# Kernel optimization log

Hardware: AMD Instinct MI355X
Metric: run time of the kernel (lower is better)

## Reference

```python
import jax, jax.numpy as jnp
import numpy as np
import math

D_MODEL = 768
NUM_HEADS = 12


def setup_inputs() -> dict:
    key = jax.random.key(0)
    ks = jax.random.split(key, 5)
    B, S, D = 2, 2048, D_MODEL
    scale = 1.0 / math.sqrt(D)
    x = jax.random.normal(ks[0], (B, S, D), dtype=jnp.float32)
    Wq = jax.random.normal(ks[1], (D, D), dtype=jnp.float32) * scale
    Wk = jax.random.normal(ks[2], (D, D), dtype=jnp.float32) * scale
    Wv = jax.random.normal(ks[3], (D, D), dtype=jnp.float32) * scale
    Wo = jax.random.normal(ks[4], (D, D), dtype=jnp.float32) * scale
    return {"x": x, "Wq": Wq, "Wk": Wk, "Wv": Wv, "Wo": Wo}


def _mhsa(x, Wq, Wk, Wv, Wo):
    B, S, D = x.shape
    H = NUM_HEADS
    hd = D // H
    # Linear(in, out) with weight [out, in]: y = x @ W^T
    q = x @ Wq.T
    k = x @ Wk.T
    v = x @ Wv.T
    # [B, S, H, hd] -> [B, H, S, hd]
    q = q.reshape(B, S, H, hd).transpose(0, 2, 1, 3)
    k = k.reshape(B, S, H, hd).transpose(0, 2, 1, 3)
    v = v.reshape(B, S, H, hd).transpose(0, 2, 1, 3)
    scores = jnp.einsum("bhqd,bhkd->bhqk", q, k) / jnp.sqrt(jnp.float32(hd))
    causal = jnp.tril(jnp.ones((S, S), dtype=bool))  # True where allowed
    scores = jnp.where(causal, scores, -jnp.inf)
    probs = jax.nn.softmax(scores, axis=-1)
    o = jnp.einsum("bhqk,bhkd->bhqd", probs, v)
    o = o.transpose(0, 2, 1, 3).reshape(B, S, D)
    return o @ Wo.T


def reference(x, Wq, Wk, Wv, Wo):
    return _mhsa(x, Wq, Wk, Wv, Wo)
```

## Files before the change

### kernel.cpp

```cpp
#include <hip/hip_runtime.h>
#include <math.h>

#define NHEAD 12
#define HD    64
#define SEQ   2048
#define BATCH 2
#define DM    768

typedef unsigned short u16;
typedef __attribute__((ext_vector_type(8))) short bf16x8;
typedef __attribute__((ext_vector_type(8))) unsigned short u16x8;
typedef __attribute__((ext_vector_type(4))) float f32x4;

__device__ __forceinline__ u16 f2bf(float f) {
    unsigned u = __builtin_bit_cast(unsigned, f);
    return (u16)((u + 0x7fffu + ((u >> 16) & 1u)) >> 16);
}
__device__ __forceinline__ bf16x8 as_bf16x8(uint4 v) { return __builtin_bit_cast(bf16x8, v); }
__device__ __forceinline__ u16x8  as_u16x8(uint4 v)  { return __builtin_bit_cast(u16x8, v); }
__device__ __forceinline__ f32x4 mfma16(bf16x8 a, bf16x8 b, f32x4 c) {
    return __builtin_amdgcn_mfma_f32_16x16x32_bf16(a, b, c, 0, 0, 0);
}

__global__ void cvt4(const float* __restrict__ s, u16* __restrict__ d, int n4) {
    int i = blockIdx.x * blockDim.x + threadIdx.x;
    if (i < n4) {
        float4 v = ((const float4*)s)[i];
        ushort4 o;
        o.x = f2bf(v.x); o.y = f2bf(v.y); o.z = f2bf(v.z); o.w = f2bf(v.w);
        ((ushort4*)d)[i] = o;
    }
}

__global__ __launch_bounds__(256)
void qkv_mfma(const u16* __restrict__ X,
              const u16* __restrict__ Wq, const u16* __restrict__ Wk,
              const u16* __restrict__ Wv,
              u16* __restrict__ Q, u16* __restrict__ K, u16* __restrict__ V)
{
    const u16* W = blockIdx.z == 0 ? Wq : blockIdx.z == 1 ? Wk : Wv;
    u16*       Y = blockIdx.z == 0 ? Q  : blockIdx.z == 1 ? K  : V;
    const int m0 = blockIdx.x * 128, n0 = blockIdx.y * 128;

    __shared__ __align__(16) u16 As[128 * 40];
    __shared__ __align__(16) u16 Bs[128 * 40];

    const int tid = threadIdx.x;
    const int w = tid >> 6, l = tid & 63, lg = l >> 4, lr = l & 15;
    const int wr = w >> 1, wc = w & 1;
    const int srow = tid >> 1, sh = tid & 1;

    const u16* ga = X + (size_t)(m0 + srow) * DM + sh * 16;
    const u16* gb = W + (size_t)(n0 + srow) * DM + sh * 16;
    const int sidx = srow * 40 + sh * 16;

    f32x4 acc[4][4];
    #pragma unroll
    for (int i = 0; i < 4; ++i)
        #pragma unroll
        for (int j = 0; j < 4; ++j) acc[i][j] = (f32x4){0.f, 0.f, 0.f, 0.f};

    for (int k0 = 0; k0 < DM; k0 += 32) {
        uint4 a0 = *(const uint4*)(ga + k0);
        uint4 a1 = *(const uint4*)(ga + k0 + 8);
        uint4 b0 = *(const uint4*)(gb + k0);
        uint4 b1 = *(const uint4*)(gb + k0 + 8);
        __syncthreads();
        *(uint4*)&As[sidx] = a0; *(uint4*)&As[sidx + 8] = a1;
        *(uint4*)&Bs[sidx] = b0; *(uint4*)&Bs[sidx + 8] = b1;
        __syncthreads();
        bf16x8 af[4], bfr[4];
        #pragma unroll
        for (int i = 0; i < 4; ++i) {
            af[i]  = as_bf16x8(*(const uint4*)&As[(wr * 64 + i * 16 + lr) * 40 + lg * 8]);
            bfr[i] = as_bf16x8(*(const uint4*)&Bs[(wc * 64 + i * 16 + lr) * 40 + lg * 8]);
        }
        #pragma unroll
        for (int i = 0; i < 4; ++i)
            #pragma unroll
            for (int j = 0; j < 4; ++j)
                acc[i][j] = mfma16(af[i], bfr[j], acc[i][j]);
    }

    #pragma unroll
    for (int i = 0; i < 4; ++i) {
        const int mb = m0 + wr * 64 + i * 16 + lg * 4;
        #pragma unroll
        for (int j = 0; j < 4; ++j) {
            const int n = n0 + wc * 64 + j * 16 + lr;
            const int h = n >> 6, dc = n & 63;
            #pragma unroll
            for (int r = 0; r < 4; ++r) {
                const int m = mb + r;
                const int b = m >> 11, s2 = m & 2047;
                Y[(((size_t)b * NHEAD + h) * SEQ + s2) * HD + dc] = f2bf(acc[i][j][r]);
            }
        }
    }
}

__global__ __launch_bounds__(128)
void attn_mfma(const u16* __restrict__ Qg, const u16* __restrict__ Kg,
               const u16* __restrict__ Vg, u16* __restrict__ Og)
{
    const int p  = blockIdx.x;
    const int bh = blockIdx.y;
    const size_t base = (size_t)bh * SEQ * HD;
    const u16* Qb = Qg + base;
    const u16* Kb = Kg + base;
    const u16* Vb = Vg + base;
    u16*       Ob = Og + base;

    __shared__ __align__(16) u16 Ks[64 * 64];
    __shared__ __align__(16) u16 Vt[64 * 64];
    __shared__ __align__(16) u16 Ps[2 * 16 * 64];

    const int tid = threadIdx.x;
    const int w = tid >> 6, l = tid & 63, lg = l >> 4, lr = l & 15;

    const int qb0 = p * 32;
    const int qb1 = (63 - p) * 32;
    const int ke0 = (qb0 + 31) >> 6;
    const int ke1 = (qb1 + 31) >> 6;

    bf16x8 qf[2][2];
    #pragma unroll
    for (int sub = 0; sub < 2; ++sub) {
        const int qrow = (sub ? qb1 : qb0) + w * 16 + lr;
        #pragma unroll
        for (int kh = 0; kh < 2; ++kh)
            qf[sub][kh] = as_bf16x8(*(const uint4*)(Qb + (size_t)qrow * HD + kh * 32 + lg * 8));
    }

    float ms[2][4], ls[2][4];
    f32x4 ov[2][4];
    #pragma unroll
    for (int sub = 0; sub < 2; ++sub)
        #pragma unroll
        for (int r = 0; r < 4; ++r) {
            ms[sub][r] = -INFINITY; ls[sub][r] = 0.f;
            ov[sub][r] = (f32x4){0.f, 0.f, 0.f, 0.f};
        }

    const int srow = l;
    const int hb   = w;

    for (int kt = 0; kt <= ke1; ++kt) {
        const int k0 = kt * 64;

        const u16* kp = Kb + (size_t)(k0 + srow) * HD + hb * 32;
        const u16* vp = Vb + (size_t)(k0 + srow) * HD + hb * 32;
        uint4 kq[4], vq[4];
        #pragma unroll
        for (int q = 0; q < 4; ++q) kq[q] = *(const uint4*)(kp + q * 8);
        #pragma unroll
        for (int q = 0; q < 4; ++q) vq[q] = *(const uint4*)(vp + q * 8);

        __syncthreads();
        #pragma unroll
        for (int q = 0; q < 4; ++q) {
            const int cb = hb * 64 + q * 16;
            *(uint4*)&Ks[srow * 64 + ((cb ^ ((srow & 7) << 4)) >> 1)] = kq[q];
        }
        #pragma unroll
        for (int q = 0; q < 4; ++q) {
            u16x8 vv = as_u16x8(vq[q]);
            #pragma unroll
            for (int e = 0; e < 8; ++e) {
                const int d = hb * 32 + q * 8 + e;
                Vt[d * 64 + (((srow * 2) ^ ((d & 7) << 4)) >> 1)] = vv[e];
            }
        }
        __syncthreads();

        #pragma unroll
        for (int sub = 0; sub < 2; ++sub) {
            const int qbase = sub ? qb1 : qb0;
            const int kend  = sub ? ke1 : ke0;
            if (kt > kend) continue;

            f32x4 sc[4];
            #pragma unroll
            for (int nj = 0; nj < 4; ++nj) sc[nj] = (f32x4){0.f, 0.f, 0.f, 0.f};
            #pragma unroll
            for (int kh = 0; kh < 2; ++kh) {
                #pragma unroll
                for (int nj = 0; nj < 4; ++nj) {
                    const int s  = nj * 16 + lr;
                    const int cb = lg * 16 + kh * 64;
                    bf16x8 kf = as_bf16x8(*(const uint4*)&Ks[s * 64 + ((cb ^ ((s & 7) << 4)) >> 1)]);
                    sc[nj] = mfma16(qf[sub][kh], kf, sc[nj]);
                }
            }

            const bool lastt = (kt == kend);
            #pragma unroll
            for (int nj = 0; nj < 4; ++nj) {
                const int kk = k0 + nj * 16 + lr;
                #pragma unroll
                for (int r = 0; r < 4; ++r) {
                    float v = sc[nj][r] * 0.125f;
                    if (lastt) {
                        const int qrow = qbase + w * 16 + lg * 4 + r;
                        if (kk > qrow) v = -INFINITY;
                    }
                    sc[nj][r] = v;
                }
            }

            float fac[4];
            #pragma unroll
            for (int r = 0; r < 4; ++r) {
                float rm = fmaxf(fmaxf(sc[0][r], sc[1][r]), fmaxf(sc[2][r], sc[3][r]));
                rm = fmaxf(rm, __shfl_xor(rm, 1));
                rm = fmaxf(rm, __shfl_xor(rm, 2));
                rm = fmaxf(rm, __shfl_xor(rm, 4));
                rm = fmaxf(rm, __shfl_xor(rm, 8));
                const float mo = ms[sub][r];
                const float mn = fmaxf(mo, rm);
                const float f  = __expf(mo - mn);
                ms[sub][r] = mn; fac[r] = f;
                float rs = 0.f;
                #pragma unroll
                for (int nj = 0; nj < 4; ++nj) {
                    const float pv = __expf(sc[nj][r] - mn);
                    sc[nj][r] = pv;
                    rs += pv;
                }
                rs += __shfl_xor(rs, 1); rs += __shfl_xor(rs, 2);
                rs += __shfl_xor(rs, 4); rs += __shfl_xor(rs, 8);
                ls[sub][r] = ls[sub][r] * f + rs;
            }

            #pragma unroll
            for (int dj = 0; dj < 4; ++dj)
                #pragma unroll
                for (int r = 0; r < 4; ++r)
                    ov[sub][dj][r] *= fac[r];
            #pragma unroll
            for (int nj = 0; nj < 4; ++nj)
                #pragma unroll
                for (int r = 0; r < 4; ++r) {
                    const int row = lg * 4 + r, col = nj * 16 + lr;
                    Ps[w * 1024 + row * 64 + (((col * 2) ^ ((row & 7) << 4)) >> 1)] = f2bf(sc[nj][r]);
                }

            #pragma unroll
            for (int ks = 0; ks < 2; ++ks) {
                const int cb = lg * 16 + ks * 64;
                bf16x8 pa = as_bf16x8(*(const uint4*)&Ps[w * 1024 + lr * 64 + ((cb ^ ((lr & 7) << 4)) >> 1)]);
                #pragma unroll
                for (int dj = 0; dj < 4; ++dj) {
                    const int d = dj * 16 + lr;
                    bf16x8 vf = as_bf16x8(*(const uint4*)&Vt[d * 64 + ((cb ^ ((d & 7) << 4)) >> 1)]);
                    ov[sub][dj] = mfma16(pa, vf, ov[sub][dj]);
                }
            }
        }
    }

    #pragma unroll
    for (int sub = 0; sub < 2; ++sub) {
        const int qbase = sub ? qb1 : qb0;
        #pragma unroll
        for (int r = 0; r < 4; ++r) {
            const float inv = 1.0f / ls[sub][r];
            const int row = qbase + w * 16 + lg * 4 + r;
            #pragma unroll
            for (int dj = 0; dj < 4; ++dj)
                Ob[(size_t)row * HD + dj * 16 + lr] = f2bf(ov[sub][dj][r] * inv);
        }
    }
}

__global__ __launch_bounds__(256)
void proj_mfma(const u16* __restrict__ O, const u16* __restrict__ Wo,
               float* __restrict__ out)
{
    const int m0 = blockIdx.x * 128, n0 = blockIdx.y * 128;

    __shared__ __align__(16) u16 As[128 * 40];
    __shared__ __align__(16) u16 Bs[128 * 40];

    const int tid = threadIdx.x;
    const int w = tid >> 6, l = tid & 63, lg = l >> 4, lr = l & 15;
    const int wr = w >> 1, wc = w & 1;
    const int srow = tid >> 1, sh = tid & 1;

    const int m = m0 + srow;
    const int b = m >> 11, s2 = m & 2047;
    const u16* gb = Wo + (size_t)(n0 + srow) * DM + sh * 16;
    const int sidx = srow * 40 + sh * 16;

    f32x4 acc[4][4];
    #pragma unroll
    for (int i = 0; i < 4; ++i)
        #pragma unroll
        for (int j = 0; j < 4; ++j) acc[i][j] = (f32x4){0.f, 0.f, 0.f, 0.f};

    for (int k0 = 0; k0 < DM; k0 += 32) {
        const int kk = k0 + sh * 16;
        const u16* ga = O + (((size_t)b * NHEAD + (kk >> 6)) * SEQ + s2) * HD + (kk & 63);
        uint4 a0 = *(const uint4*)(ga);
        uint4 a1 = *(const uint4*)(ga + 8);
        uint4 b0 = *(const uint4*)(gb + k0);
        uint4 b1 = *(const uint4*)(gb + k0 + 8);
        __syncthreads();
        *(uint4*)&As[sidx] = a0; *(uint4*)&As[sidx + 8] = a1;
        *(uint4*)&Bs[sidx] = b0; *(uint4*)&Bs[sidx + 8] = b1;
        __syncthreads();
        bf16x8 af[4], bfr[4];
        #pragma unroll
        for (int i = 0; i < 4; ++i) {
            af[i]  = as_bf16x8(*(const uint4*)&As[(wr * 64 + i * 16 + lr) * 40 + lg * 8]);
            bfr[i] = as_bf16x8(*(const uint4*)&Bs[(wc * 64 + i * 16 + lr) * 40 + lg * 8]);
        }
        #pragma unroll
        for (int i = 0; i < 4; ++i)
            #pragma unroll
            for (int j = 0; j < 4; ++j)
                acc[i][j] = mfma16(af[i], bfr[j], acc[i][j]);
    }

    #pragma unroll
    for (int i = 0; i < 4; ++i) {
        const int mb = m0 + wr * 64 + i * 16 + lg * 4;
        #pragma unroll
        for (int j = 0; j < 4; ++j) {
            const int n = n0 + wc * 64 + j * 16 + lr;
            #pragma unroll
            for (int r = 0; r < 4; ++r)
                out[(size_t)(mb + r) * DM + n] = acc[i][j][r];
        }
    }
}

extern "C" void kernel_launch(void* const* d_in, const int* in_sizes, int n_in,
                              void* d_out, int out_size, void* d_ws, size_t ws_size,
                              hipStream_t stream)
{
    const float* x  = (const float*)d_in[0];
    const float* Wq = (const float*)d_in[1];
    const float* Wk = (const float*)d_in[2];
    const float* Wv = (const float*)d_in[3];
    const float* Wo = (const float*)d_in[4];
    float* out = (float*)d_out;

    const size_t nx = (size_t)BATCH * SEQ * DM;
    const size_t nw = (size_t)DM * DM;
    const size_t nh = (size_t)BATCH * NHEAD * SEQ * HD;

    u16* xb  = (u16*)d_ws;
    u16* wqb = xb  + nx;
    u16* wkb = wqb + nw;
    u16* wvb = wkb + nw;
    u16* wob = wvb + nw;
    u16* Qb  = wob + nw;
    u16* Kb  = Qb  + nh;
    u16* Vb  = Kb  + nh;
    u16* Ob  = Vb  + nh;

    cvt4<<<(int)(nx / 4 / 256), 256, 0, stream>>>(x,  xb,  (int)(nx / 4));
    cvt4<<<(int)(nw / 4 / 256), 256, 0, stream>>>(Wq, wqb, (int)(nw / 4));
    cvt4<<<(int)(nw / 4 / 256), 256, 0, stream>>>(Wk, wkb, (int)(nw / 4));
    cvt4<<<(int)(nw / 4 / 256), 256, 0, stream>>>(Wv, wvb, (int)(nw / 4));
    cvt4<<<(int)(nw / 4 / 256), 256, 0, stream>>>(Wo, wob, (int)(nw / 4));

    dim3 g1(BATCH * SEQ / 128, DM / 128, 3);
    qkv_mfma<<<g1, 256, 0, stream>>>(xb, wqb, wkb, wvb, Qb, Kb, Vb);

    dim3 g2(32, BATCH * NHEAD);
    attn_mfma<<<g2, 128, 0, stream>>>(Qb, Kb, Vb, Ob);

    dim3 g3(BATCH * SEQ / 128, DM / 128);
    proj_mfma<<<g3, 256, 0, stream>>>(Ob, wob, out);
}
```

Baseline: 236.5 us.

## Restructure attention blocks to 64 query rows, merge weight casts, add MFMA priority

The attention kernel drops the paired-tile scheme (two 32-row query tiles from opposite ends of the causal triangle per 128-thread block) in favour of one contiguous 64-row tile per 256-thread block. Blocks are launched heaviest-first, and the V transpose swizzle is changed to reduce LDS bank conflicts. The four weight-conversion launches become a single launch, and s_setprio raises wave priority around the MFMA loops in all three kernels. In exchange, per-block work is no longer balanced across the causal mask, which risks tail imbalance, though the reversed ordering is meant to offset it.

```diff
diff --git a/kernel.cpp b/kernel.cpp
--- a/kernel.cpp
+++ b/kernel.cpp
@@ -23,6 +23,21 @@
 }
 
 __global__ void cvt4(const float* __restrict__ s, u16* __restrict__ d, int n4) {
+    int i = blockIdx.x * blockDim.x + threadIdx.x;
+    if (i < n4) {
+        float4 v = ((const float4*)s)[i];
+        ushort4 o;
+        o.x = f2bf(v.x); o.y = f2bf(v.y); o.z = f2bf(v.z); o.w = f2bf(v.w);
+        ((ushort4*)d)[i] = o;
+    }
+}
+
+__global__ void cvt4w(const float* __restrict__ s0, const float* __restrict__ s1,
+                      const float* __restrict__ s2, const float* __restrict__ s3,
+                      u16* __restrict__ d0, u16* __restrict__ d1,
+                      u16* __restrict__ d2, u16* __restrict__ d3, int n4) {
+    const float* s = blockIdx.y == 0 ? s0 : blockIdx.y == 1 ? s1 : blockIdx.y == 2 ? s2 : s3;
+    u16*         d = blockIdx.y == 0 ? d0 : blockIdx.y == 1 ? d1 : blockIdx.y == 2 ? d2 : d3;
     int i = blockIdx.x * blockDim.x + threadIdx.x;
     if (i < n4) {
         float4 v = ((const float4*)s)[i];
@@ -75,11 +90,13 @@
             af[i]  = as_bf16x8(*(const uint4*)&As[(wr * 64 + i * 16 + lr) * 40 + lg * 8]);
             bfr[i] = as_bf16x8(*(const uint4*)&Bs[(wc * 64 + i * 16 + lr) * 40 + lg * 8]);
         }
+        __builtin_amdgcn_s_setprio(1);
         #pragma unroll
         for (int i = 0; i < 4; ++i)
             #pragma unroll
             for (int j = 0; j < 4; ++j)
                 acc[i][j] = mfma16(af[i], bfr[j], acc[i][j]);
+        __builtin_amdgcn_s_setprio(0);
     }
 
     #pragma unroll
@@ -99,12 +116,13 @@
     }
 }
 
-__global__ __launch_bounds__(128)
+__global__ __launch_bounds__(256)
 void attn_mfma(const u16* __restrict__ Qg, const u16* __restrict__ Kg,
                const u16* __restrict__ Vg, u16* __restrict__ Og)
 {
-    const int p  = blockIdx.x;
+    const int q0 = (31 - blockIdx.x) * 64;
     const int bh = blockIdx.y;
+    const int kend = q0 >> 6;
     const size_t base = (size_t)bh * SEQ * HD;
     const u16* Qb = Qg + base;
     const u16* Kb = Kg + base;
@@ -113,163 +131,143 @@
 
     __shared__ __align__(16) u16 Ks[64 * 64];
     __shared__ __align__(16) u16 Vt[64 * 64];
-    __shared__ __align__(16) u16 Ps[2 * 16 * 64];
+    __shared__ __align__(16) u16 Ps[4 * 16 * 64];
 
     const int tid = threadIdx.x;
     const int w = tid >> 6, l = tid & 63, lg = l >> 4, lr = l & 15;
 
-    const int qb0 = p * 32;
-    const int qb1 = (63 - p) * 32;
-    const int ke0 = (qb0 + 31) >> 6;
-    const int ke1 = (qb1 + 31) >> 6;
-
-    bf16x8 qf[2][2];
-    #pragma unroll
-    for (int sub = 0; sub < 2; ++sub) {
-        const int qrow = (sub ? qb1 : qb0) + w * 16 + lr;
-        #pragma unroll
-        for (int kh = 0; kh < 2; ++kh)
-            qf[sub][kh] = as_bf16x8(*(const uint4*)(Qb + (size_t)qrow * HD + kh * 32 + lg * 8));
-    }
-
-    float ms[2][4], ls[2][4];
-    f32x4 ov[2][4];
-    #pragma unroll
-    for (int sub = 0; sub < 2; ++sub)
+    const int srow = w * 16 + (l >> 2);
+    const int c0   = (l & 3) * 16;
+
+    const int qrow = q0 + w * 16 + lr;
+    bf16x8 qf[2];
+    #pragma unroll
+    for (int kh = 0; kh < 2; ++kh)
+        qf[kh] = as_bf16x8(*(const uint4*)(Qb + (size_t)qrow * HD + kh * 32 + lg * 8));
+
+    float ms[4], ls[4];
+    f32x4 ov[4];
+    #pragma unroll
+    for (int r = 0; r < 4; ++r) { ms[r] = -INFINITY; ls[r] = 0.f; }
+    #pragma unroll
+    for (int dj = 0; dj < 4; ++dj) ov[dj] = (f32x4){0.f, 0.f, 0.f, 0.f};
+
+    for (int kt = 0; kt <= kend; ++kt) {
+        const int k0 = kt * 64;
+
+        const u16* kp = Kb + (size_t)(k0 + srow) * HD + c0;
+        const u16* vp = Vb + (size_t)(k0 + srow) * HD + c0;
+        uint4 kq0 = *(const uint4*)(kp);
+        uint4 kq1 = *(const uint4*)(kp + 8);
+        uint4 vq0 = *(const uint4*)(vp);
+        uint4 vq1 = *(const uint4*)(vp + 8);
+
+        __syncthreads();
+        {
+            const int sw = (srow & 7) << 4;
+            *(uint4*)&Ks[srow * 64 + (((c0 * 2) ^ sw) >> 1)]        = kq0;
+            *(uint4*)&Ks[srow * 64 + ((((c0 + 8) * 2) ^ sw) >> 1)]  = kq1;
+        }
+        #pragma unroll
+        for (int h = 0; h < 2; ++h) {
+            u16x8 vv = as_u16x8(h ? vq1 : vq0);
+            #pragma unroll
+            for (int e = 0; e < 8; ++e) {
+                const int d  = c0 + h * 8 + e;
+                const int cs = (d & 7) ^ ((d >> 3) & 7);
+                Vt[d * 64 + (((srow * 2) ^ (cs << 4)) >> 1)] = vv[e];
+            }
+        }
+        __syncthreads();
+
+        f32x4 sc[4];
+        #pragma unroll
+        for (int nj = 0; nj < 4; ++nj) sc[nj] = (f32x4){0.f, 0.f, 0.f, 0.f};
+        __builtin_amdgcn_s_setprio(1);
+        #pragma unroll
+        for (int kh = 0; kh < 2; ++kh) {
+            #pragma unroll
+            for (int nj = 0; nj < 4; ++nj) {
+                const int s  = nj * 16 + lr;
+                const int cb = kh * 64 + lg * 16;
+                bf16x8 kf = as_bf16x8(*(const uint4*)&Ks[s * 64 + ((cb ^ ((s & 7) << 4)) >> 1)]);
+                sc[nj] = mfma16(qf[kh], kf, sc[nj]);
+            }
+        }
+        __builtin_amdgcn_s_setprio(0);
+
+        const bool lastt = (kt == kend);
+        #pragma unroll
+        for (int nj = 0; nj < 4; ++nj) {
+            const int kk = k0 + nj * 16 + lr;
+            #pragma unroll
+            for (int r = 0; r < 4; ++r) {
+                float v = sc[nj][r] * 0.125f;
+                if (lastt && kk > (q0 + w * 16 + lg * 4 + r)) v = -INFINITY;
+                sc[nj][r] = v;
+            }
+        }
+
+        float fac[4];
         #pragma unroll
         for (int r = 0; r < 4; ++r) {
-            ms[sub][r] = -INFINITY; ls[sub][r] = 0.f;
-            ov[sub][r] = (f32x4){0.f, 0.f, 0.f, 0.f};
-        }
-
-    const int srow = l;
-    const int hb   = w;
-
-    for (int kt = 0; kt <= ke1; ++kt) {
-        const int k0 = kt * 64;
-
-        const u16* kp = Kb + (size_t)(k0 + srow) * HD + hb * 32;
-        const u16* vp = Vb + (size_t)(k0 + srow) * HD + hb * 32;
-        uint4 kq[4], vq[4];
-        #pragma unroll
-        for (int q = 0; q < 4; ++q) kq[q] = *(const uint4*)(kp + q * 8);
-        #pragma unroll
-        for (int q = 0; q < 4; ++q) vq[q] = *(const uint4*)(vp + q * 8);
-
-        __syncthreads();
-        #pragma unroll
-        for (int q = 0; q < 4; ++q) {
-            const int cb = hb * 64 + q * 16;
-            *(uint4*)&Ks[srow * 64 + ((cb ^ ((srow & 7) << 4)) >> 1)] = kq[q];
-        }
-        #pragma unroll
-        for (int q = 0; q < 4; ++q) {
-            u16x8 vv = as_u16x8(vq[q]);
-            #pragma unroll
-            for (int e = 0; e < 8; ++e) {
-                const int d = hb * 32 + q * 8 + e;
-                Vt[d * 64 + (((srow * 2) ^ ((d & 7) << 4)) >> 1)] = vv[e];
-            }
-        }
-        __syncthreads();
-
-        #pragma unroll
-        for (int sub = 0; sub < 2; ++sub) {
-            const int qbase = sub ? qb1 : qb0;
-            const int kend  = sub ? ke1 : ke0;
-            if (kt > kend) continue;
-
-            f32x4 sc[4];
-            #pragma unroll
-            for (int nj = 0; nj < 4; ++nj) sc[nj] = (f32x4){0.f, 0.f, 0.f, 0.f};
-            #pragma unroll
-            for (int kh = 0; kh < 2; ++kh) {
-                #pragma unroll
-                for (int nj = 0; nj < 4; ++nj) {
-                    const int s  = nj * 16 + lr;
-                    const int cb = lg * 16 + kh * 64;
-                    bf16x8 kf = as_bf16x8(*(const uint4*)&Ks[s * 64 + ((cb ^ ((s & 7) << 4)) >> 1)]);
-                    sc[nj] = mfma16(qf[sub][kh], kf, sc[nj]);
-                }
-            }
-
-            const bool lastt = (kt == kend);
+            float rm = fmaxf(fmaxf(sc[0][r], sc[1][r]), fmaxf(sc[2][r], sc[3][r]));
+            rm = fmaxf(rm, __shfl_xor(rm, 1));
+            rm = fmaxf(rm, __shfl_xor(rm, 2));
+            rm = fmaxf(rm, __shfl_xor(rm, 4));
+            rm = fmaxf(rm, __shfl_xor(rm, 8));
+            const float mo = ms[r];
+            const float mn = fmaxf(mo, rm);
+            const float f  = __expf(mo - mn);
+            ms[r] = mn; fac[r] = f;
+            float rs = 0.f;
             #pragma unroll
             for (int nj = 0; nj < 4; ++nj) {
-                const int kk = k0 + nj * 16 + lr;
-                #pragma unroll
-                for (int r = 0; r < 4; ++r) {
-                    float v = sc[nj][r] * 0.125f;
-                    if (lastt) {
-                        const int qrow = qbase + w * 16 + lg * 4 + r;
-                        if (kk > qrow) v = -INFINITY;
-                    }
-                    sc[nj][r] = v;
-                }
-            }
-
-            float fac[4];
+                const float pv = __expf(sc[nj][r] - mn);
+                sc[nj][r] = pv;
+                rs += pv;
+            }
+            rs += __shfl_xor(rs, 1); rs += __shfl_xor(rs, 2);
+            rs += __shfl_xor(rs, 4); rs += __shfl_xor(rs, 8);
+            ls[r] = ls[r] * f + rs;
+        }
+
+        #pragma unroll
+        for (int dj = 0; dj < 4; ++dj)
+            #pragma unroll
+            for (int r = 0; r < 4; ++r)
+                ov[dj][r] *= fac[r];
+        #pragma unroll
+        for (int nj = 0; nj < 4; ++nj)
             #pragma unroll
             for (int r = 0; r < 4; ++r) {
-                float rm = fmaxf(fmaxf(sc[0][r], sc[1][r]), fmaxf(sc[2][r], sc[3][r]));
-                rm = fmaxf(rm, __shfl_xor(rm, 1));
-                rm = fmaxf(rm, __shfl_xor(rm, 2));
-                rm = fmaxf(rm, __shfl_xor(rm, 4));
-                rm = fmaxf(rm, __shfl_xor(rm, 8));
-                const float mo = ms[sub][r];
-                const float mn = fmaxf(mo, rm);
-                const float f  = __expf(mo - mn);
-                ms[sub][r] = mn; fac[r] = f;
-                float rs = 0.f;
-                #pragma unroll
-                for (int nj = 0; nj < 4; ++nj) {
-                    const float pv = __expf(sc[nj][r] - mn);
-                    sc[nj][r] = pv;
-                    rs += pv;
-                }
-                rs += __shfl_xor(rs, 1); rs += __shfl_xor(rs, 2);
-                rs += __shfl_xor(rs, 4); rs += __shfl_xor(rs, 8);
-                ls[sub][r] = ls[sub][r] * f + rs;
-            }
-
-            #pragma unroll
-            for (int dj = 0; dj < 4; ++dj)
-                #pragma unroll
-                for (int r = 0; r < 4; ++r)
-                    ov[sub][dj][r] *= fac[r];
-            #pragma unroll
-            for (int nj = 0; nj < 4; ++nj)
-                #pragma unroll
-                for (int r = 0; r < 4; ++r) {
-                    const int row = lg * 4 + r, col = nj * 16 + lr;
-                    Ps[w * 1024 + row * 64 + (((col * 2) ^ ((row & 7) << 4)) >> 1)] = f2bf(sc[nj][r]);
-                }
-
-            #pragma unroll
-            for (int ks = 0; ks < 2; ++ks) {
-                const int cb = lg * 16 + ks * 64;
-                bf16x8 pa = as_bf16x8(*(const uint4*)&Ps[w * 1024 + lr * 64 + ((cb ^ ((lr & 7) << 4)) >> 1)]);
-                #pragma unroll
-                for (int dj = 0; dj < 4; ++dj) {
-                    const int d = dj * 16 + lr;
-                    bf16x8 vf = as_bf16x8(*(const uint4*)&Vt[d * 64 + ((cb ^ ((d & 7) << 4)) >> 1)]);
-                    ov[sub][dj] = mfma16(pa, vf, ov[sub][dj]);
-                }
-            }
-        }
-    }
-
-    #pragma unroll
-    for (int sub = 0; sub < 2; ++sub) {
-        const int qbase = sub ? qb1 : qb0;
-        #pragma unroll
-        for (int r = 0; r < 4; ++r) {
-            const float inv = 1.0f / ls[sub][r];
-            const int row = qbase + w * 16 + lg * 4 + r;
-            #pragma unroll
-            for (int dj = 0; dj < 4; ++dj)
-                Ob[(size_t)row * HD + dj * 16 + lr] = f2bf(ov[sub][dj][r] * inv);
-        }
+                const int row = lg * 4 + r, col = nj * 16 + lr;
+                Ps[w * 1024 + row * 64 + (((col * 2) ^ ((row & 7) << 4)) >> 1)] = f2bf(sc[nj][r]);
+            }
+
+        __builtin_amdgcn_s_setprio(1);
+        #pragma unroll
+        for (int ks = 0; ks < 2; ++ks) {
+            const int cb = ks * 64 + lg * 16;
+            bf16x8 pa = as_bf16x8(*(const uint4*)&Ps[w * 1024 + lr * 64 + ((cb ^ ((lr & 7) << 4)) >> 1)]);
+            #pragma unroll
+            for (int dj = 0; dj < 4; ++dj) {
+                const int d  = dj * 16 + lr;
+                const int cs = (d & 7) ^ ((d >> 3) & 7);
+                bf16x8 vf = as_bf16x8(*(const uint4*)&Vt[d * 64 + ((cb ^ (cs << 4)) >> 1)]);
+                ov[dj] = mfma16(pa, vf, ov[dj]);
+            }
+        }
+        __builtin_amdgcn_s_setprio(0);
+    }
+
+    #pragma unroll
+    for (int r = 0; r < 4; ++r) {
+        const float inv = 1.0f / ls[r];
+        const int row = q0 + w * 16 + lg * 4 + r;
+        #pragma unroll
+        for (int dj = 0; dj < 4; ++dj)
+            Ob[(size_t)row * HD + dj * 16 + lr] = f2bf(ov[dj][r] * inv);
     }
 }
 
@@ -315,11 +313,13 @@
             af[i]  = as_bf16x8(*(const uint4*)&As[(wr * 64 + i * 16 + lr) * 40 + lg * 8]);
             bfr[i] = as_bf16x8(*(const uint4*)&Bs[(wc * 64 + i * 16 + lr) * 40 + lg * 8]);
         }
+        __builtin_amdgcn_s_setprio(1);
         #pragma unroll
         for (int i = 0; i < 4; ++i)
             #pragma unroll
             for (int j = 0; j < 4; ++j)
                 acc[i][j] = mfma16(af[i], bfr[j], acc[i][j]);
+        __builtin_amdgcn_s_setprio(0);
     }
 
     #pragma unroll
@@ -360,17 +360,15 @@
     u16* Vb  = Kb  + nh;
     u16* Ob  = Vb  + nh;
 
-    cvt4<<<(int)(nx / 4 / 256), 256, 0, stream>>>(x,  xb,  (int)(nx / 4));
-    cvt4<<<(int)(nw / 4 / 256), 256, 0, stream>>>(Wq, wqb, (int)(nw / 4));
-    cvt4<<<(int)(nw / 4 / 256), 256, 0, stream>>>(Wk, wkb, (int)(nw / 4));
-    cvt4<<<(int)(nw / 4 / 256), 256, 0, stream>>>(Wv, wvb, (int)(nw / 4));
-    cvt4<<<(int)(nw / 4 / 256), 256, 0, stream>>>(Wo, wob, (int)(nw / 4));
+    cvt4<<<(int)(nx / 4 / 256), 256, 0, stream>>>(x, xb, (int)(nx / 4));
+    dim3 gw((unsigned)(nw / 4 / 256), 4);
+    cvt4w<<<gw, 256, 0, stream>>>(Wq, Wk, Wv, Wo, wqb, wkb, wvb, wob, (int)(nw / 4));
 
     dim3 g1(BATCH * SEQ / 128, DM / 128, 3);
     qkv_mfma<<<g1, 256, 0, stream>>>(xb, wqb, wkb, wvb, Qb, Kb, Vb);
 
     dim3 g2(32, BATCH * NHEAD);
-    attn_mfma<<<g2, 128, 0, stream>>>(Qb, Kb, Vb, Ob);
+    attn_mfma<<<g2, 256, 0, stream>>>(Qb, Kb, Vb, Ob);
 
     dim3 g3(BATCH * SEQ / 128, DM / 128);
     proj_mfma<<<g3, 256, 0, stream>>>(Ob, wob, out);
```

Measured after the change: 216.5 us. 1.09x faster.
